# Kernel tuning notes

Hardware: AMD Instinct MI355X
Metric: run time of the kernel (lower is better)

The kernel has to match this reference:

```python
import jax, jax.numpy as jnp
import numpy as np
from jax import lax

N = 8192      # nodes == batch (forward cats node and batch embeddings)
E = 262144    # edges, avg degree 32
T = 32        # seq_len
DD = 16       # dynamic_feature_dim
DS = 128      # static_feature_dim
GH = 64       # gnn_hidden_dim
RH = 128      # rnn_hidden_dim
L = 10        # output_lead_times
EPS = 1e-5


def setup_inputs() -> dict:
    key = jax.random.key(0)
    ks = jax.random.split(key, 32)
    def rn(i, shape, s=0.05):
        return jax.random.normal(ks[i], shape, jnp.float32) * s
    return {
        "dynamic_features": rn(0, (N, T, DD), 1.0),
        "x_static": rn(1, (N, DS), 1.0),
        "edge_index": jax.random.randint(ks[2], (2, E), 0, N, jnp.int32),
        "gcn1_w": rn(3, (DS, GH)), "gcn1_b": rn(4, (GH,)),
        "gcn2_w": rn(5, (GH, GH)), "gcn2_b": rn(6, (GH,)),
        "bn1_g": 1.0 + rn(7, (GH,)), "bn1_b": rn(8, (GH,)),
        "bn2_g": 1.0 + rn(9, (GH,)), "bn2_b": rn(10, (GH,)),
        "w_ih0": rn(11, (4 * RH, DD)), "w_hh0": rn(12, (4 * RH, RH)),
        "b_ih0": rn(13, (4 * RH,)), "b_hh0": rn(14, (4 * RH,)),
        "w_ih1": rn(15, (4 * RH, RH)), "w_hh1": rn(16, (4 * RH, RH)),
        "b_ih1": rn(17, (4 * RH,)), "b_hh1": rn(18, (4 * RH,)),
        "fc1_w": rn(19, (GH + RH, 128)), "fc1_b": rn(20, (128,)),
        "fbn_g": 1.0 + rn(21, (128,)), "fbn_b": rn(22, (128,)),
        "fc2_w": rn(23, (128, 64)), "fc2_b": rn(24, (64,)),
        "out_w": rn(25, (64, L)), "out_b": rn(26, (L,)),
    }


def _gcn(x, w, b, src, dst, n):
    h = x @ w
    loops = jnp.arange(n, dtype=src.dtype)
    s = jnp.concatenate([src, loops])
    d = jnp.concatenate([dst, loops])
    deg = jax.ops.segment_sum(jnp.ones(s.shape[0], x.dtype), d, num_segments=n)
    dis = lax.rsqrt(jnp.maximum(deg, 1.0))
    msg = h[s] * (dis[s] * dis[d])[:, None]
    return jax.ops.segment_sum(msg, d, num_segments=n) + b


def _bn(x, g, b):
    # eval-mode BatchNorm1d: running_mean=0, running_var=1
    return x * (g * lax.rsqrt(jnp.asarray(1.0 + EPS, x.dtype))) + b


def _lstm_layer(xp, w_hh):
    # xp: [B, T, 4H] input projection with both biases already added
    B = xp.shape[0]
    H = w_hh.shape[1]
    h0 = jnp.zeros((B, H), xp.dtype)
    c0 = jnp.zeros((B, H), xp.dtype)
    def step(carry, xt):
        h, c = carry
        gates = xt + h @ w_hh.T  # torch gate order: i, f, g, o
        i, f, g, o = jnp.split(gates, 4, axis=-1)
        c = jax.nn.sigmoid(f) * c + jax.nn.sigmoid(i) * jnp.tanh(g)
        h = jax.nn.sigmoid(o) * jnp.tanh(c)
        return (h, c), h
    _, hs = lax.scan(step, (h0, c0), jnp.swapaxes(xp, 0, 1))
    return jnp.swapaxes(hs, 0, 1)  # [B, T, H]


def _forward(dynamic_features, x_static, edge_index,
             gcn1_w, gcn1_b, gcn2_w, gcn2_b, bn1_g, bn1_b, bn2_g, bn2_b,
             w_ih0, w_hh0, b_ih0, b_hh0, w_ih1, w_hh1, b_ih1, b_hh1,
             fc1_w, fc1_b, fbn_g, fbn_b, fc2_w, fc2_b, out_w, out_b):
    src, dst = edge_index[0], edge_index[1]
    n = x_static.shape[0]
    # GNN branch (dropout = eval-mode identity)
    h = _gcn(x_static, gcn1_w, gcn1_b, src, dst, n)
    h = jax.nn.relu(_bn(h, bn1_g, bn1_b))
    h = _gcn(h, gcn2_w, gcn2_b, src, dst, n)
    gnn_emb = jax.nn.relu(_bn(h, bn2_g, bn2_b))
    # 2-layer LSTM branch
    xp0 = jnp.einsum('btd,gd->btg', dynamic_features, w_ih0) + b_ih0 + b_hh0
    h1 = _lstm_layer(xp0, w_hh0)
    xp1 = jnp.einsum('bth,gh->btg', h1, w_ih1) + b_ih1 + b_hh1
    h2 = _lstm_layer(xp1, w_hh1)
    rnn_emb = h2[:, -1, :]
    # fusion MLP
    fused = jnp.concatenate([gnn_emb, rnn_emb], axis=1)
    x = jax.nn.relu(_bn(fused @ fc1_w + fc1_b, fbn_g, fbn_b))
    x = jax.nn.relu(x @ fc2_w + fc2_b)
    return x @ out_w + out_b


def reference(dynamic_features, x_static, edge_index,
              gcn1_w, gcn1_b, gcn2_w, gcn2_b, bn1_g, bn1_b, bn2_g, bn2_b,
              w_ih0, w_hh0, b_ih0, b_hh0, w_ih1, w_hh1, b_ih1, b_hh1,
              fc1_w, fc1_b, fbn_g, fbn_b, fc2_w, fc2_b, out_w, out_b):
    return _forward(dynamic_features, x_static, edge_index,
                    gcn1_w, gcn1_b, gcn2_w, gcn2_b, bn1_g, bn1_b, bn2_g, bn2_b,
                    w_ih0, w_hh0, b_ih0, b_hh0, w_ih1, w_hh1, b_ih1, b_hh1,
                    fc1_w, fc1_b, fbn_g, fbn_b, fc2_w, fc2_b, out_w, out_b)
```

## Files before the change

kernel.cpp:

```cpp
#include <hip/hip_runtime.h>
#include <hip/hip_bf16.h>

#define NN 8192
#define NE 262144

typedef float v2 __attribute__((ext_vector_type(2)));
typedef float v4 __attribute__((ext_vector_type(4)));
typedef float f4 __attribute__((ext_vector_type(4)));
typedef _Float16 h8 __attribute__((ext_vector_type(8)));
typedef _Float16 h4 __attribute__((ext_vector_type(4)));

__device__ __forceinline__ float rcp_(float x) { return __builtin_amdgcn_rcpf(x); }
__device__ __forceinline__ float sigm(float x) { return rcp_(1.0f + __expf(-x)); }
__device__ __forceinline__ float tanh_(float x) { return 1.0f - 2.0f * rcp_(__expf(2.0f * x) + 1.0f); }

__global__ void k_prep(const float* __restrict__ wih0, const float* __restrict__ whh0,
                       const float* __restrict__ bih0, const float* __restrict__ bhh0,
                       const float* __restrict__ wih1, const float* __restrict__ whh1,
                       const float* __restrict__ bih1, const float* __restrict__ bhh1,
                       _Float16* __restrict__ WB0h, _Float16* __restrict__ TLg,
                       _Float16* __restrict__ WB1, float* __restrict__ bias) {
    int i = blockIdx.x * 256 + threadIdx.x;
    if (i < 65536) {
        int idx = i & 7, col = (i >> 3) & 511, kgq = (i >> 12) & 3, kt = i >> 14;
        int kh = kt * 32 + kgq * 8 + idx;
        WB0h[i] = (_Float16)whh0[col * 128 + kh];
    } else if (i < 73728) {
        int m = i - 65536;
        int kd = m & 15, g = m >> 4;
        TLg[m] = (_Float16)wih0[g * 16 + kd];
    } else if (i < 204800) {
        int m = i - 73728;
        int kt = m >> 14, rem = m & 16383, g = rem >> 5, kk = rem & 31, k = kt * 32 + kk;
        WB1[m] = (_Float16)((k < 128) ? wih1[g * 128 + k] : whh1[g * 128 + (k - 128)]);
    } else if (i < 205824) {
        int g = i - 204800;
        bias[g] = (g < 512) ? (bih0[g] + bhh0[g]) : (bih1[g - 512] + bhh1[g - 512]);
    }
}
__global__ void k_cvt_dyn(const float* __restrict__ dyn, _Float16* __restrict__ dyn16) {
    int i = blockIdx.x * 256 + threadIdx.x;
    f4 v = *(const f4*)(dyn + (size_t)i * 4);
    h4 o = {(_Float16)v[0], (_Float16)v[1], (_Float16)v[2], (_Float16)v[3]};
    *(h4*)(dyn16 + (size_t)i * 4) = o;
}

__global__ void k_deg_count(const int* __restrict__ dst, int* __restrict__ cnt) {
    int i = blockIdx.x * 256 + threadIdx.x;
    if (i < NE) atomicAdd(&cnt[dst[i]], 1);
}
__global__ __launch_bounds__(1024) void k_scan(const int* __restrict__ cnt, int* __restrict__ rowstart,
                                               float* __restrict__ dis) {
    __shared__ int part[1024];
    int t = threadIdx.x;
    int base = t * 8, s = 0, loc[8];
#pragma unroll
    for (int i = 0; i < 8; ++i) { loc[i] = s; s += cnt[base + i]; }
    part[t] = s;
    __syncthreads();
    for (int off = 1; off < 1024; off <<= 1) {
        int v = part[t];
        int add = (t >= off) ? part[t - off] : 0;
        __syncthreads();
        part[t] = v + add;
        __syncthreads();
    }
    int pre = (t == 0) ? 0 : part[t - 1];
#pragma unroll
    for (int i = 0; i < 8; ++i) {
        rowstart[base + i] = pre + loc[i];
        dis[base + i] = rsqrtf((float)(cnt[base + i] + 1));
    }
    if (t == 1023) rowstart[8192] = NE;
}
__global__ void k_fill(const int* __restrict__ src, const int* __restrict__ dst,
                       const int* __restrict__ rowstart, int* __restrict__ cursor,
                       int* __restrict__ srcidx) {
    int e = blockIdx.x * 256 + threadIdx.x;
    if (e < NE) {
        int d = dst[e];
        int pos = rowstart[d] + atomicAdd(&cursor[d], 1);
        srcidx[pos] = src[e];
    }
}
__global__ __launch_bounds__(256) void k_gcn_gemm(const float* __restrict__ in, const float* __restrict__ w,
                                                  const float* __restrict__ dis, float* __restrict__ hs, int K) {
    int wv = threadIdx.x >> 6, ln = threadIdx.x & 63;
    int row = blockIdx.x * 4 + wv;
    const float* xp = in + (size_t)row * K;
    float a = 0.f;
#pragma unroll 4
    for (int k = 0; k < K; ++k) a += xp[k] * w[k * 64 + ln];
    hs[(size_t)row * 64 + ln] = a * dis[row];
}
__global__ __launch_bounds__(256) void k_gather(const float* __restrict__ hs, const int* __restrict__ srcidx,
                                                const int* __restrict__ rowstart, const float* __restrict__ dis,
                                                const float* __restrict__ gb, const float* __restrict__ bng,
                                                const float* __restrict__ bnb, float* __restrict__ out) {
    int ln = threadIdx.x & 63;
    int d = (blockIdx.x * 256 + threadIdx.x) >> 6;
    float acc = hs[(size_t)d * 64 + ln];
    int b = rowstart[d], e = rowstart[d + 1];
    int i = b;
    for (; i + 4 <= e; i += 4) {
        int s0 = srcidx[i], s1 = srcidx[i + 1], s2 = srcidx[i + 2], s3 = srcidx[i + 3];
        acc += hs[(size_t)s0 * 64 + ln];
        acc += hs[(size_t)s1 * 64 + ln];
        acc += hs[(size_t)s2 * 64 + ln];
        acc += hs[(size_t)s3 * 64 + ln];
    }
    for (; i < e; ++i) acc += hs[(size_t)srcidx[i] * 64 + ln];
    float rs = rsqrtf(1.0f + 1e-5f);
    float v = acc * dis[d] + gb[ln];
    v = v * (bng[ln] * rs) + bnb[ln];
    out[(size_t)d * 64 + ln] = fmaxf(v, 0.f);
}

__device__ __forceinline__ h8 ldx(const _Float16* xs, int buf, int row, int chunk) {
    return *(const h8*)((const char*)xs + buf * 16384 + row * 512 + ((chunk ^ (row & 7)) << 4));
}
__device__ __forceinline__ void wrx(_Float16* xs, int buf, int row, int col, _Float16 v) {
    *(_Float16*)((char*)xs + buf * 16384 + row * 512 + ((((col >> 3) ^ (row & 7))) << 4) + (col & 7) * 2) = v;
}

__global__ __launch_bounds__(512, 2) void k_lstm(const _Float16* __restrict__ dyn16,
                                                 const _Float16* __restrict__ WB0h,
                                                 const _Float16* __restrict__ TLg,
                                                 const _Float16* __restrict__ WB1,
                                                 const float* __restrict__ bias,
                                                 float* __restrict__ rnn) {
    __shared__ __align__(16) _Float16 wb0[65536];
    __shared__ __align__(16) _Float16 xs[16384];

    const int tid = threadIdx.x;
    const int wv = tid >> 6, ln = tid & 63;
    const int lr = ln & 15, kg = ln >> 4;
    const int j = wv * 16 + lr;
    const int row0 = blockIdx.x * 32;

    for (int i = tid; i < 8192; i += 512) ((v4*)wb0)[i] = ((const v4*)WB0h)[i];
    for (int i = tid; i < 16384; i += 512) xs[i] = (_Float16)0.f;

    h8 b1r[8][4];
#pragma unroll
    for (int kt = 0; kt < 8; ++kt)
#pragma unroll
        for (int q = 0; q < 4; ++q)
            b1r[kt][q] = *(const h8*)(WB1 + (size_t)kt * 16384 + (q * 128 + j) * 32 + kg * 8);
    h8 bt[4];
#pragma unroll
    for (int q = 0; q < 4; ++q)
        bt[q] = *(const h8*)(TLg + (q * 128 + j) * 16 + (kg & 1) * 8);

    float b0q[4], b1q[4];
#pragma unroll
    for (int q = 0; q < 4; ++q) { b0q[q] = bias[q * 128 + j]; b1q[q] = bias[512 + q * 128 + j]; }
    float c0[2][4], c1[2][4];
#pragma unroll
    for (int mt = 0; mt < 2; ++mt)
#pragma unroll
        for (int r = 0; r < 4; ++r) { c0[mt][r] = 0.f; c1[mt][r] = 0.f; }

    h8 dreg[2];
#pragma unroll
    for (int mt = 0; mt < 2; ++mt)
#pragma unroll
        for (int e = 0; e < 8; ++e) dreg[mt][e] = (_Float16)0.f;
    if (kg < 2) {
#pragma unroll
        for (int mt = 0; mt < 2; ++mt)
            dreg[mt] = *(const h8*)(dyn16 + (size_t)(row0 + mt * 16 + lr) * 512 + (kg & 1) * 8);
    }
    __syncthreads();

    {
        f4 acc[2][4];
#pragma unroll
        for (int q = 0; q < 4; ++q) { f4 z = {b0q[q], b0q[q], b0q[q], b0q[q]}; acc[0][q] = z; acc[1][q] = z; }
#pragma unroll
        for (int q = 0; q < 4; ++q) {
            acc[0][q] = __builtin_amdgcn_mfma_f32_16x16x32_f16(dreg[0], bt[q], acc[0][q], 0, 0, 0);
            acc[1][q] = __builtin_amdgcn_mfma_f32_16x16x32_f16(dreg[1], bt[q], acc[1][q], 0, 0, 0);
        }
#pragma unroll
        for (int mt = 0; mt < 2; ++mt)
#pragma unroll
            for (int r = 0; r < 4; ++r) {
                float iv = acc[mt][0][r], fv = acc[mt][1][r], gv = acc[mt][2][r], ov = acc[mt][3][r];
                float c = sigm(fv) * c0[mt][r] + sigm(iv) * tanh_(gv);
                c0[mt][r] = c;
                wrx(xs, 0, mt * 16 + kg * 4 + r, j, (_Float16)(sigm(ov) * tanh_(c)));
            }
        if (kg < 2) {
#pragma unroll
            for (int mt = 0; mt < 2; ++mt)
                dreg[mt] = *(const h8*)(dyn16 + (size_t)(row0 + mt * 16 + lr) * 512 + 16 + (kg & 1) * 8);
        }
    }

#pragma unroll 1
    for (int i = 0; i < 31; ++i) {
        const int cur = i & 1, old = cur ^ 1;
        __syncthreads();
        f4 acc[2][4];
#pragma unroll
        for (int q = 0; q < 4; ++q) { f4 z = {b1q[q], b1q[q], b1q[q], b1q[q]}; acc[0][q] = z; acc[1][q] = z; }
#pragma unroll
        for (int kt = 0; kt < 8; ++kt) {
            const int bufA = (kt < 4) ? cur : old;
            const int ch = (kt < 4) ? (kt * 4 + kg) : (16 + (kt - 4) * 4 + kg);
            h8 a0 = ldx(xs, bufA, lr, ch);
            h8 a1 = ldx(xs, bufA, 16 + lr, ch);
#pragma unroll
            for (int q = 0; q < 4; ++q) {
                acc[0][q] = __builtin_amdgcn_mfma_f32_16x16x32_f16(a0, b1r[kt][q], acc[0][q], 0, 0, 0);
                acc[1][q] = __builtin_amdgcn_mfma_f32_16x16x32_f16(a1, b1r[kt][q], acc[1][q], 0, 0, 0);
            }
        }
#pragma unroll
        for (int mt = 0; mt < 2; ++mt)
#pragma unroll
            for (int r = 0; r < 4; ++r) {
                float iv = acc[mt][0][r], fv = acc[mt][1][r], gv = acc[mt][2][r], ov = acc[mt][3][r];
                float c = sigm(fv) * c1[mt][r] + sigm(iv) * tanh_(gv);
                c1[mt][r] = c;
                wrx(xs, cur, mt * 16 + kg * 4 + r, 128 + j, (_Float16)(sigm(ov) * tanh_(c)));
            }
#pragma unroll
        for (int q = 0; q < 4; ++q) { f4 z = {b0q[q], b0q[q], b0q[q], b0q[q]}; acc[0][q] = z; acc[1][q] = z; }
#pragma unroll
        for (int kt = 0; kt < 4; ++kt) {
            h8 a0 = ldx(xs, cur, lr, kt * 4 + kg);
            h8 a1 = ldx(xs, cur, 16 + lr, kt * 4 + kg);
            h8 bq[4];
#pragma unroll
            for (int q = 0; q < 4; ++q)
                bq[q] = *(const h8*)(wb0 + (size_t)(((kt * 4 + kg) * 512 + q * 128 + j) * 8));
#pragma unroll
            for (int q = 0; q < 4; ++q) {
                acc[0][q] = __builtin_amdgcn_mfma_f32_16x16x32_f16(a0, bq[q], acc[0][q], 0, 0, 0);
                acc[1][q] = __builtin_amdgcn_mfma_f32_16x16x32_f16(a1, bq[q], acc[1][q], 0, 0, 0);
            }
        }
#pragma unroll
        for (int q = 0; q < 4; ++q) {
            acc[0][q] = __builtin_amdgcn_mfma_f32_16x16x32_f16(dreg[0], bt[q], acc[0][q], 0, 0, 0);
            acc[1][q] = __builtin_amdgcn_mfma_f32_16x16x32_f16(dreg[1], bt[q], acc[1][q], 0, 0, 0);
        }
#pragma unroll
        for (int mt = 0; mt < 2; ++mt)
#pragma unroll
            for (int r = 0; r < 4; ++r) {
                float iv = acc[mt][0][r], fv = acc[mt][1][r], gv = acc[mt][2][r], ov = acc[mt][3][r];
                float c = sigm(fv) * c0[mt][r] + sigm(iv) * tanh_(gv);
                c0[mt][r] = c;
                wrx(xs, old, mt * 16 + kg * 4 + r, j, (_Float16)(sigm(ov) * tanh_(c)));
            }
        if (i < 30 && kg < 2) {
#pragma unroll
            for (int mt = 0; mt < 2; ++mt)
                dreg[mt] = *(const h8*)(dyn16 + (size_t)(row0 + mt * 16 + lr) * 512 + (i + 2) * 16 + (kg & 1) * 8);
        }
    }
    __syncthreads();
    {
        const int cur = 1, old = 0;
        f4 acc[2][4];
#pragma unroll
        for (int q = 0; q < 4; ++q) { f4 z = {b1q[q], b1q[q], b1q[q], b1q[q]}; acc[0][q] = z; acc[1][q] = z; }
#pragma unroll
        for (int kt = 0; kt < 8; ++kt) {
            const int bufA = (kt < 4) ? cur : old;
            const int ch = (kt < 4) ? (kt * 4 + kg) : (16 + (kt - 4) * 4 + kg);
            h8 a0 = ldx(xs, bufA, lr, ch);
            h8 a1 = ldx(xs, bufA, 16 + lr, ch);
#pragma unroll
            for (int q = 0; q < 4; ++q) {
                acc[0][q] = __builtin_amdgcn_mfma_f32_16x16x32_f16(a0, b1r[kt][q], acc[0][q], 0, 0, 0);
                acc[1][q] = __builtin_amdgcn_mfma_f32_16x16x32_f16(a1, b1r[kt][q], acc[1][q], 0, 0, 0);
            }
        }
#pragma unroll
        for (int mt = 0; mt < 2; ++mt)
#pragma unroll
            for (int r = 0; r < 4; ++r) {
                float iv = acc[mt][0][r], fv = acc[mt][1][r], gv = acc[mt][2][r], ov = acc[mt][3][r];
                float c = sigm(fv) * c1[mt][r] + sigm(iv) * tanh_(gv);
                float h = sigm(ov) * tanh_(c);
                rnn[(size_t)(row0 + mt * 16 + kg * 4 + r) * 128 + j] = h;
            }
    }
}

__global__ __launch_bounds__(256) void k_head(const float* __restrict__ gnn, const float* __restrict__ rnn,
                                              const float* __restrict__ fc1w, const float* __restrict__ fc1b,
                                              const float* __restrict__ fbng, const float* __restrict__ fbnb,
                                              const float* __restrict__ fc2w, const float* __restrict__ fc2b,
                                              const float* __restrict__ outw, const float* __restrict__ outb,
                                              float* __restrict__ out) {
    __shared__ __align__(16) float xin[32][196];
    __shared__ __align__(16) float xh2[32][132];
    __shared__ __align__(16) float xh3[32][68];
    const int tid = threadIdx.x;
    const int r0 = blockIdx.x * 32;
    for (int i = tid; i < 32 * 64; i += 256) { int r = i >> 6, c = i & 63; xin[r][c] = gnn[(size_t)(r0 + r) * 64 + c]; }
    for (int i = tid; i < 32 * 128; i += 256) { int r = i >> 7, c = i & 127; xin[r][64 + c] = rnn[(size_t)(r0 + r) * 128 + c]; }
    __syncthreads();
    const int wv = tid >> 6, ln = tid & 63, wr = wv * 8;
    const float rs = rsqrtf(1.0f + 1e-5f);
    float a[8][2];
    float b0 = fc1b[2 * ln], b1 = fc1b[2 * ln + 1];
#pragma unroll
    for (int r = 0; r < 8; ++r) { a[r][0] = b0; a[r][1] = b1; }
    for (int k = 0; k < 192; ++k) {
        v2 w = *(const v2*)&fc1w[k * 128 + 2 * ln];
#pragma unroll
        for (int r = 0; r < 8; ++r) { float x = xin[wr + r][k]; a[r][0] += x * w[0]; a[r][1] += x * w[1]; }
    }
    float s0 = fbng[2 * ln] * rs, s1 = fbng[2 * ln + 1] * rs;
    float bb0 = fbnb[2 * ln], bb1 = fbnb[2 * ln + 1];
#pragma unroll
    for (int r = 0; r < 8; ++r) {
        v2 h;
        h[0] = fmaxf(a[r][0] * s0 + bb0, 0.f);
        h[1] = fmaxf(a[r][1] * s1 + bb1, 0.f);
        *(v2*)&xh2[wr + r][2 * ln] = h;
    }
    __syncthreads();
    float a2[8];
    float b2 = fc2b[ln];
#pragma unroll
    for (int r = 0; r < 8; ++r) a2[r] = b2;
    for (int k = 0; k < 128; ++k) {
        float w = fc2w[k * 64 + ln];
#pragma unroll
        for (int r = 0; r < 8; ++r) a2[r] += xh2[wr + r][k] * w;
    }
#pragma unroll
    for (int r = 0; r < 8; ++r) xh3[wr + r][ln] = fmaxf(a2[r], 0.f);
    __syncthreads();
    if (ln < 10) {
#pragma unroll
        for (int r = 0; r < 8; ++r) {
            float a3 = outb[ln];
            for (int k = 0; k < 64; ++k) a3 += xh3[wr + r][k] * outw[k * 10 + ln];
            out[(size_t)(r0 + wr + r) * 10 + ln] = a3;
        }
    }
}

extern "C" void kernel_launch(void* const* d_in, const int* in_sizes, int n_in,
                              void* d_out, int out_size, void* d_ws, size_t ws_size,
                              hipStream_t stream) {
    const float* dyn  = (const float*)d_in[0];
    const float* xs_  = (const float*)d_in[1];
    const int*   ei   = (const int*)d_in[2];
    const float* g1w  = (const float*)d_in[3];
    const float* g1b  = (const float*)d_in[4];
    const float* g2w  = (const float*)d_in[5];
    const float* g2b  = (const float*)d_in[6];
    const float* bn1g = (const float*)d_in[7];
    const float* bn1b = (const float*)d_in[8];
    const float* bn2g = (const float*)d_in[9];
    const float* bn2b = (const float*)d_in[10];
    const float* wih0 = (const float*)d_in[11];
    const float* whh0 = (const float*)d_in[12];
    const float* bih0 = (const float*)d_in[13];
    const float* bhh0 = (const float*)d_in[14];
    const float* wih1 = (const float*)d_in[15];
    const float* whh1 = (const float*)d_in[16];
    const float* bih1 = (const float*)d_in[17];
    const float* bhh1 = (const float*)d_in[18];
    const float* fc1w = (const float*)d_in[19];
    const float* fc1b = (const float*)d_in[20];
    const float* fbng = (const float*)d_in[21];
    const float* fbnb = (const float*)d_in[22];
    const float* fc2w = (const float*)d_in[23];
    const float* fc2b = (const float*)d_in[24];
    const float* outw = (const float*)d_in[25];
    const float* outb = (const float*)d_in[26];
    float* out = (float*)d_out;

    char* ws = (char*)d_ws;
    _Float16* WB0h  = (_Float16*)(ws + 0);
    _Float16* TLg   = (_Float16*)(ws + 131072);
    _Float16* WB1   = (_Float16*)(ws + 147456);
    _Float16* dyn16 = (_Float16*)(ws + 409600);
    float* fbase = (float*)(ws + 8798208);
    float* bias = fbase;
    float* dis  = fbase + 1024;
    float* hs   = fbase + 9216;
    float* y1   = fbase + 533504;
    float* gnn  = fbase + 1057792;
    float* rnn  = fbase + 1582080;
    int* ibase   = (int*)(ws + 19320832);
    int* cnt     = ibase;
    int* cursor  = ibase + 8192;
    int* rowstart= ibase + 16384;
    int* srcidx  = ibase + 24592;

    const int* srcp = ei;
    const int* dstp = ei + NE;

    k_prep<<<804, 256, 0, stream>>>(wih0, whh0, bih0, bhh0, wih1, whh1, bih1, bhh1, WB0h, TLg, WB1, bias);
    k_cvt_dyn<<<4096, 256, 0, stream>>>(dyn, dyn16);
    hipMemsetAsync(cnt, 0, 2 * 8192 * sizeof(int), stream);
    k_deg_count<<<1024, 256, 0, stream>>>(dstp, cnt);
    k_scan<<<1, 1024, 0, stream>>>(cnt, rowstart, dis);
    k_fill<<<1024, 256, 0, stream>>>(srcp, dstp, rowstart, cursor, srcidx);
    k_gcn_gemm<<<2048, 256, 0, stream>>>(xs_, g1w, dis, hs, 128);
    k_gather<<<2048, 256, 0, stream>>>(hs, srcidx, rowstart, dis, g1b, bn1g, bn1b, y1);
    k_gcn_gemm<<<2048, 256, 0, stream>>>(y1, g2w, dis, hs, 64);
    k_gather<<<2048, 256, 0, stream>>>(hs, srcidx, rowstart, dis, g2b, bn2g, bn2b, gnn);
    k_lstm<<<256, 512, 0, stream>>>(dyn16, WB0h, TLg, WB1, bias, rnn);
    k_head<<<256, 256, 0, stream>>>(gnn, rnn, fc1w, fc1b, fbng, fbnb, fc2w, fc2b, outw, outb, out);
}
```

Before: 295.3 us.

## Fuse prep kernels, fuse GCN gather with second GEMM, cheaper LSTM gate math

```diff
diff --git a/kernel.cpp b/kernel.cpp
--- a/kernel.cpp
+++ b/kernel.cpp
@@ -11,44 +11,55 @@
 typedef _Float16 h4 __attribute__((ext_vector_type(4)));
 
 __device__ __forceinline__ float rcp_(float x) { return __builtin_amdgcn_rcpf(x); }
-__device__ __forceinline__ float sigm(float x) { return rcp_(1.0f + __expf(-x)); }
-__device__ __forceinline__ float tanh_(float x) { return 1.0f - 2.0f * rcp_(__expf(2.0f * x) + 1.0f); }
-
-__global__ void k_prep(const float* __restrict__ wih0, const float* __restrict__ whh0,
-                       const float* __restrict__ bih0, const float* __restrict__ bhh0,
-                       const float* __restrict__ wih1, const float* __restrict__ whh1,
-                       const float* __restrict__ bih1, const float* __restrict__ bhh1,
-                       _Float16* __restrict__ WB0h, _Float16* __restrict__ TLg,
-                       _Float16* __restrict__ WB1, float* __restrict__ bias) {
-    int i = blockIdx.x * 256 + threadIdx.x;
-    if (i < 65536) {
-        int idx = i & 7, col = (i >> 3) & 511, kgq = (i >> 12) & 3, kt = i >> 14;
-        int kh = kt * 32 + kgq * 8 + idx;
-        WB0h[i] = (_Float16)whh0[col * 128 + kh];
-    } else if (i < 73728) {
-        int m = i - 65536;
-        int kd = m & 15, g = m >> 4;
-        TLg[m] = (_Float16)wih0[g * 16 + kd];
-    } else if (i < 204800) {
-        int m = i - 73728;
-        int kt = m >> 14, rem = m & 16383, g = rem >> 5, kk = rem & 31, k = kt * 32 + kk;
-        WB1[m] = (_Float16)((k < 128) ? wih1[g * 128 + k] : whh1[g * 128 + (k - 128)]);
-    } else if (i < 205824) {
-        int g = i - 204800;
-        bias[g] = (g < 512) ? (bih0[g] + bhh0[g]) : (bih1[g - 512] + bhh1[g - 512]);
-    }
-}
-__global__ void k_cvt_dyn(const float* __restrict__ dyn, _Float16* __restrict__ dyn16) {
-    int i = blockIdx.x * 256 + threadIdx.x;
-    f4 v = *(const f4*)(dyn + (size_t)i * 4);
-    h4 o = {(_Float16)v[0], (_Float16)v[1], (_Float16)v[2], (_Float16)v[3]};
-    *(h4*)(dyn16 + (size_t)i * 4) = o;
-}
-
-__global__ void k_deg_count(const int* __restrict__ dst, int* __restrict__ cnt) {
-    int i = blockIdx.x * 256 + threadIdx.x;
-    if (i < NE) atomicAdd(&cnt[dst[i]], 1);
-}
+__device__ __forceinline__ float ew(float iv, float fv, float gv, float ov, float& c) {
+    float F = __expf(-fv);
+    float I = __expf(-iv);
+    float G = __expf(2.0f * gv);
+    c = c * rcp_(1.0f + F) + (G - 1.0f) * rcp_((G + 1.0f) * (1.0f + I));
+    float O = __expf(-ov);
+    float E = __expf(2.0f * c);
+    return (E - 1.0f) * rcp_((E + 1.0f) * (1.0f + O));
+}
+
+__global__ void k_prep_all(const float* __restrict__ dyn,
+                           const float* __restrict__ wih0, const float* __restrict__ whh0,
+                           const float* __restrict__ bih0, const float* __restrict__ bhh0,
+                           const float* __restrict__ wih1, const float* __restrict__ whh1,
+                           const float* __restrict__ bih1, const float* __restrict__ bhh1,
+                           const int* __restrict__ dst,
+                           _Float16* __restrict__ dyn16, _Float16* __restrict__ WB0h,
+                           _Float16* __restrict__ TLg, _Float16* __restrict__ WB1,
+                           float* __restrict__ bias, int* __restrict__ cnt) {
+    int b = blockIdx.x, tid = threadIdx.x;
+    if (b < 4096) {
+        int i = b * 256 + tid;
+        f4 v = *(const f4*)(dyn + (size_t)i * 4);
+        h4 o = {(_Float16)v[0], (_Float16)v[1], (_Float16)v[2], (_Float16)v[3]};
+        *(h4*)(dyn16 + (size_t)i * 4) = o;
+    } else if (b < 4900) {
+        int i = (b - 4096) * 256 + tid;
+        if (i < 65536) {
+            int idx = i & 7, col = (i >> 3) & 511, kgq = (i >> 12) & 3, kt = i >> 14;
+            int kh = kt * 32 + kgq * 8 + idx;
+            WB0h[i] = (_Float16)whh0[col * 128 + kh];
+        } else if (i < 73728) {
+            int m = i - 65536;
+            int kd = m & 15, g = m >> 4;
+            TLg[m] = (_Float16)wih0[g * 16 + kd];
+        } else if (i < 204800) {
+            int m = i - 73728;
+            int kt = m >> 14, rem = m & 16383, g = rem >> 5, kk = rem & 31, k = kt * 32 + kk;
+            WB1[m] = (_Float16)((k < 128) ? wih1[g * 128 + k] : whh1[g * 128 + (k - 128)]);
+        } else {
+            int g = i - 204800;
+            bias[g] = (g < 512) ? (bih0[g] + bhh0[g]) : (bih1[g - 512] + bhh1[g - 512]);
+        }
+    } else {
+        int e = (b - 4900) * 256 + tid;
+        if (e < NE) atomicAdd(&cnt[dst[e]], 1);
+    }
+}
+
 __global__ __launch_bounds__(1024) void k_scan(const int* __restrict__ cnt, int* __restrict__ rowstart,
                                                float* __restrict__ dis) {
     __shared__ int part[1024];
@@ -92,6 +103,32 @@
 #pragma unroll 4
     for (int k = 0; k < K; ++k) a += xp[k] * w[k * 64 + ln];
     hs[(size_t)row * 64 + ln] = a * dis[row];
+}
+__global__ __launch_bounds__(256) void k_gather_gemm(const float* __restrict__ hs, const int* __restrict__ srcidx,
+                                                     const int* __restrict__ rowstart, const float* __restrict__ dis,
+                                                     const float* __restrict__ gb, const float* __restrict__ bng,
+                                                     const float* __restrict__ bnb, const float* __restrict__ g2w,
+                                                     float* __restrict__ hs2) {
+    int ln = threadIdx.x & 63;
+    int d = (blockIdx.x * 256 + threadIdx.x) >> 6;
+    float acc = hs[(size_t)d * 64 + ln];
+    int b = rowstart[d], e = rowstart[d + 1];
+    int i = b;
+    for (; i + 4 <= e; i += 4) {
+        int s0 = srcidx[i], s1 = srcidx[i + 1], s2 = srcidx[i + 2], s3 = srcidx[i + 3];
+        acc += hs[(size_t)s0 * 64 + ln];
+        acc += hs[(size_t)s1 * 64 + ln];
+        acc += hs[(size_t)s2 * 64 + ln];
+        acc += hs[(size_t)s3 * 64 + ln];
+    }
+    for (; i < e; ++i) acc += hs[(size_t)srcidx[i] * 64 + ln];
+    float rs = rsqrtf(1.0f + 1e-5f);
+    float y = acc * dis[d] + gb[ln];
+    y = fmaxf(y * (bng[ln] * rs) + bnb[ln], 0.f);
+    float a2 = 0.f;
+#pragma unroll 8
+    for (int k = 0; k < 64; ++k) a2 += __shfl(y, k, 64) * g2w[k * 64 + ln];
+    hs2[(size_t)d * 64 + ln] = a2 * dis[d];
 }
 __global__ __launch_bounds__(256) void k_gather(const float* __restrict__ hs, const int* __restrict__ srcidx,
                                                 const int* __restrict__ rowstart, const float* __restrict__ dis,
@@ -186,10 +223,8 @@
         for (int mt = 0; mt < 2; ++mt)
 #pragma unroll
             for (int r = 0; r < 4; ++r) {
-                float iv = acc[mt][0][r], fv = acc[mt][1][r], gv = acc[mt][2][r], ov = acc[mt][3][r];
-                float c = sigm(fv) * c0[mt][r] + sigm(iv) * tanh_(gv);
-                c0[mt][r] = c;
-                wrx(xs, 0, mt * 16 + kg * 4 + r, j, (_Float16)(sigm(ov) * tanh_(c)));
+                float h = ew(acc[mt][0][r], acc[mt][1][r], acc[mt][2][r], acc[mt][3][r], c0[mt][r]);
+                wrx(xs, 0, mt * 16 + kg * 4 + r, j, (_Float16)h);
             }
         if (kg < 2) {
 #pragma unroll
@@ -221,10 +256,8 @@
         for (int mt = 0; mt < 2; ++mt)
 #pragma unroll
             for (int r = 0; r < 4; ++r) {
-                float iv = acc[mt][0][r], fv = acc[mt][1][r], gv = acc[mt][2][r], ov = acc[mt][3][r];
-                float c = sigm(fv) * c1[mt][r] + sigm(iv) * tanh_(gv);
-                c1[mt][r] = c;
-                wrx(xs, cur, mt * 16 + kg * 4 + r, 128 + j, (_Float16)(sigm(ov) * tanh_(c)));
+                float h = ew(acc[mt][0][r], acc[mt][1][r], acc[mt][2][r], acc[mt][3][r], c1[mt][r]);
+                wrx(xs, cur, mt * 16 + kg * 4 + r, 128 + j, (_Float16)h);
             }
 #pragma unroll
         for (int q = 0; q < 4; ++q) { f4 z = {b0q[q], b0q[q], b0q[q], b0q[q]}; acc[0][q] = z; acc[1][q] = z; }
@@ -251,10 +284,8 @@
         for (int mt = 0; mt < 2; ++mt)
 #pragma unroll
             for (int r = 0; r < 4; ++r) {
-                float iv = acc[mt][0][r], fv = acc[mt][1][r], gv = acc[mt][2][r], ov = acc[mt][3][r];
-                float c = sigm(fv) * c0[mt][r] + sigm(iv) * tanh_(gv);
-                c0[mt][r] = c;
-                wrx(xs, old, mt * 16 + kg * 4 + r, j, (_Float16)(sigm(ov) * tanh_(c)));
+                float h = ew(acc[mt][0][r], acc[mt][1][r], acc[mt][2][r], acc[mt][3][r], c0[mt][r]);
+                wrx(xs, old, mt * 16 + kg * 4 + r, j, (_Float16)h);
             }
         if (i < 30 && kg < 2) {
 #pragma unroll
@@ -284,9 +315,7 @@
         for (int mt = 0; mt < 2; ++mt)
 #pragma unroll
             for (int r = 0; r < 4; ++r) {
-                float iv = acc[mt][0][r], fv = acc[mt][1][r], gv = acc[mt][2][r], ov = acc[mt][3][r];
-                float c = sigm(fv) * c1[mt][r] + sigm(iv) * tanh_(gv);
-                float h = sigm(ov) * tanh_(c);
+                float h = ew(acc[mt][0][r], acc[mt][1][r], acc[mt][2][r], acc[mt][3][r], c1[mt][r]);
                 rnn[(size_t)(row0 + mt * 16 + kg * 4 + r) * 128 + j] = h;
             }
     }
@@ -390,7 +419,7 @@
     float* bias = fbase;
     float* dis  = fbase + 1024;
     float* hs   = fbase + 9216;
-    float* y1   = fbase + 533504;
+    float* hs2  = fbase + 533504;
     float* gnn  = fbase + 1057792;
     float* rnn  = fbase + 1582080;
     int* ibase   = (int*)(ws + 19320832);
@@ -402,16 +431,14 @@
     const int* srcp = ei;
     const int* dstp = ei + NE;
 
-    k_prep<<<804, 256, 0, stream>>>(wih0, whh0, bih0, bhh0, wih1, whh1, bih1, bhh1, WB0h, TLg, WB1, bias);
-    k_cvt_dyn<<<4096, 256, 0, stream>>>(dyn, dyn16);
     hipMemsetAsync(cnt, 0, 2 * 8192 * sizeof(int), stream);
-    k_deg_count<<<1024, 256, 0, stream>>>(dstp, cnt);
+    k_prep_all<<<5924, 256, 0, stream>>>(dyn, wih0, whh0, bih0, bhh0, wih1, whh1, bih1, bhh1,
+                                         dstp, dyn16, WB0h, TLg, WB1, bias, cnt);
     k_scan<<<1, 1024, 0, stream>>>(cnt, rowstart, dis);
     k_fill<<<1024, 256, 0, stream>>>(srcp, dstp, rowstart, cursor, srcidx);
     k_gcn_gemm<<<2048, 256, 0, stream>>>(xs_, g1w, dis, hs, 128);
-    k_gather<<<2048, 256, 0, stream>>>(hs, srcidx, rowstart, dis, g1b, bn1g, bn1b, y1);
-    k_gcn_gemm<<<2048, 256, 0, stream>>>(y1, g2w, dis, hs, 64);
-    k_gather<<<2048, 256, 0, stream>>>(hs, srcidx, rowstart, dis, g2b, bn2g, bn2b, gnn);
+    k_gather_gemm<<<2048, 256, 0, stream>>>(hs, srcidx, rowstart, dis, g1b, bn1g, bn1b, g2w, hs2);
+    k_gather<<<2048, 256, 0, stream>>>(hs2, srcidx, rowstart, dis, g2b, bn2g, bn2b, gnn);
     k_lstm<<<256, 512, 0, stream>>>(dyn16, WB0h, TLg, WB1, bias, rnn);
     k_head<<<256, 256, 0, stream>>>(gnn, rnn, fc1w, fc1b, fbng, fbnb, fc2w, fc2b, outw, outb, out);
 }
```

Result: no change. 297.4 us (+0.7%).
